# Kernel tuning notes

Hardware: AMD Instinct MI355X
Metric: run time of the kernel (lower is better)

## Reference

```python
import jax, jax.numpy as jnp
import numpy as np

H = 16  # num_heads
LN_EPS = 1e-5


def setup_inputs() -> dict:
    key = jax.random.key(0)
    ks = jax.random.split(key, 12)
    B, S, HS = 2, 1024, 1024
    D = HS // H
    vocab = 2 * 512 + 1  # 2*max_relative_position + 1
    inp = {
        "q": jax.random.normal(ks[0], (B, S, HS), jnp.float32),
        "k": jax.random.normal(ks[1], (B, S, HS), jnp.float32),
        "v": jax.random.normal(ks[2], (B, S, HS), jnp.float32),
        "rel_positions": jax.random.randint(ks[3], (S, S), 0, vocab, jnp.int64),
        "Wq": jax.random.normal(ks[4], (HS, HS), jnp.float32) * 0.02,
        "bq": jnp.zeros((HS,), jnp.float32),
        "Wk": jax.random.normal(ks[5], (HS, HS), jnp.float32) * 0.02,
        "bk": jnp.zeros((HS,), jnp.float32),
        "Wv": jax.random.normal(ks[6], (HS, HS), jnp.float32) * 0.02,
        "bv": jnp.zeros((HS,), jnp.float32),
        "rel_key_emb": jax.random.normal(ks[7], (vocab, D), jnp.float32) * 0.02,
        "rel_val_emb": jax.random.normal(ks[8], (vocab, D), jnp.float32) * 0.02,
        "Wo": jax.random.normal(ks[9], (HS, HS), jnp.float32) * 0.02,
        "bo": jnp.zeros((HS,), jnp.float32),
        "ln_g": jnp.ones((HS,), jnp.float32),
        "ln_b": jnp.zeros((HS,), jnp.float32),
    }
    return inp


def _layer_norm(x, g, b):
    mu = jnp.mean(x, axis=-1, keepdims=True)
    var = jnp.mean(jnp.square(x - mu), axis=-1, keepdims=True)
    return (x - mu) * jax.lax.rsqrt(var + LN_EPS) * g + b


def reference(q, k, v, rel_positions, Wq, bq, Wk, bk, Wv, bv,
              rel_key_emb, rel_val_emb, Wo, bo, ln_g, ln_b):
    B, S, HS = q.shape
    D = HS // H
    residual = q
    # projections (torch Linear: x @ W^T + b), split heads -> (B,H,S,D)
    qh = (q @ Wq.T + bq).reshape(B, S, H, D).transpose(0, 2, 1, 3)
    kh = (k @ Wk.T + bk).reshape(B, S, H, D).transpose(0, 2, 1, 3)
    vh = (v @ Wv.T + bv).reshape(B, S, H, D).transpose(0, 2, 1, 3)
    # relative embeddings: (S,S,D)
    rk = rel_key_emb[rel_positions]
    rv = rel_val_emb[rel_positions]
    # logits: content + relative-key term (note: original has NO 1/sqrt(d) scaling)
    logits = jnp.einsum('bhqd,bhkd->bhqk', qh, kh) \
           + jnp.einsum('bhqd,qkd->bhqk', qh, rk)
    weights = jax.nn.softmax(logits, axis=-1)
    # output: content + relative-value term
    ctx = jnp.einsum('bhqk,bhkd->bhqd', weights, vh) \
        + jnp.einsum('bhqk,qkd->bhqd', weights, rv)
    out = ctx.transpose(0, 2, 1, 3).reshape(B, S, HS) @ Wo.T + bo
    out = _layer_norm(out + residual, ln_g, ln_b)
    return (out, weights)
```

## Files before the change

### kernel.cpp

```cpp
#include <hip/hip_runtime.h>
#include <hip/hip_bf16.h>
#include <stdint.h>

#define B_   2
#define S_   1024
#define HS_  1024
#define H_   16
#define D_   64
#define V_   1025
#define VP_  1056
#define BH_  32
#define RTS_S 1072
#define RVS_  66

typedef __attribute__((ext_vector_type(8))) short  short8;
typedef __attribute__((ext_vector_type(4))) short  short4v;
typedef __attribute__((ext_vector_type(4))) float  floatx4;
typedef __attribute__((ext_vector_type(4))) int    intx4;
typedef __bf16 bf16x8 __attribute__((ext_vector_type(8)));

__device__ inline short f2b(float f) {
  union { float f; uint32_t u; } c; c.f = f;
  uint32_t u = c.u;
  uint32_t r = (u + 0x7fffu + ((u >> 16) & 1u)) >> 16;
  return (short)r;
}
__device__ inline float b2f(short s) {
  union { uint32_t u; float f; } c; c.u = ((uint32_t)(uint16_t)s) << 16;
  return c.f;
}
__device__ inline short8 cvt8(const float* p) {
  const floatx4* p4 = reinterpret_cast<const floatx4*>(p);
  floatx4 x = p4[0], y = p4[1];
  short8 r;
  r[0]=f2b(x[0]); r[1]=f2b(x[1]); r[2]=f2b(x[2]); r[3]=f2b(x[3]);
  r[4]=f2b(y[0]); r[5]=f2b(y[1]); r[6]=f2b(y[2]); r[7]=f2b(y[3]);
  return r;
}
__device__ inline short8 load_s8(const short* p) {
  return *reinterpret_cast<const short8*>(p);
}
__device__ inline floatx4 mfma16(short8 a, short8 b, floatx4 c) {
  return __builtin_amdgcn_mfma_f32_16x16x32_bf16(
      __builtin_bit_cast(bf16x8, a), __builtin_bit_cast(bf16x8, b), c, 0, 0, 0);
}

__global__ __launch_bounds__(256) void k_prep(const float* __restrict__ rve,
                                              const float* __restrict__ rke,
                                              short* __restrict__ rveB,
                                              short* __restrict__ rkeB) {
  int idx = blockIdx.x * 256 + threadIdx.x;
  if (idx < V_ * D_) {
    rveB[idx] = f2b(rve[idx]);
  } else {
    int j = idx - V_ * D_;
    if (j < V_ * D_) rkeB[j] = f2b(rke[j]);
  }
}

__global__ __launch_bounds__(256) void k_proj(
    const float* __restrict__ qi, const float* __restrict__ ki, const float* __restrict__ vi,
    const float* __restrict__ Wq, const float* __restrict__ bq,
    const float* __restrict__ Wk, const float* __restrict__ bk,
    const float* __restrict__ Wv, const float* __restrict__ bv,
    short* __restrict__ qh, short* __restrict__ kh, short* __restrict__ vhT) {
  int which = blockIdx.z;
  const float* X = which == 0 ? qi : which == 1 ? ki : vi;
  const float* W = which == 0 ? Wq : which == 1 ? Wk : Wv;
  const float* bias = which == 0 ? bq : which == 1 ? bk : bv;
  int m0 = blockIdx.y * 64, n0 = blockIdx.x * 64;
  int tid = threadIdx.x, wave = tid >> 6, lane = tid & 63;
  int qd = lane >> 4, c16 = lane & 15;
  __shared__ short Wl[64][40];
  floatx4 acc[4] = {};
  int mrow = m0 + wave * 16 + c16;
  const float* arow = X + (size_t)mrow * HS_ + qd * 8;
  int sn = tid >> 2, sk = (tid & 3) * 8;
  const float* wrow = W + (size_t)(n0 + sn) * HS_ + sk;
  for (int kc = 0; kc < HS_; kc += 32) {
    short8 wsv = cvt8(wrow + kc);
    *reinterpret_cast<short8*>(&Wl[sn][sk]) = wsv;
    __syncthreads();
    short8 a = cvt8(arow + kc);
#pragma unroll
    for (int nt = 0; nt < 4; nt++) {
      short8 b = *reinterpret_cast<const short8*>(&Wl[nt * 16 + c16][qd * 8]);
      acc[nt] = mfma16(a, b, acc[nt]);
    }
    __syncthreads();
  }
#pragma unroll
  for (int nt = 0; nt < 4; nt++) {
    int col = n0 + nt * 16 + c16;
    float bsum = bias[col];
    if (which < 2) {
      short* dst = which == 0 ? qh : kh;
#pragma unroll
      for (int r = 0; r < 4; r++) {
        int row = m0 + wave * 16 + qd * 4 + r;
        dst[(size_t)row * HS_ + col] = f2b(acc[nt][r] + bsum);
      }
    } else {
      int h = col >> 6, d = col & 63;
      int srow = m0 + wave * 16 + qd * 4;
      int bb = srow >> 10, s = srow & 1023;
      short4v pk;
#pragma unroll
      for (int r = 0; r < 4; r++) pk[r] = f2b(acc[nt][r] + bsum);
      *reinterpret_cast<short4v*>(&vhT[(((size_t)(bb * H_ + h)) * D_ + d) * S_ + s]) = pk;
    }
  }
}

__global__ __launch_bounds__(256, 4) void k_score(
    const short* __restrict__ qh, const short* __restrict__ kh,
    const short* __restrict__ rkeB, const int* __restrict__ rp,
    float* __restrict__ weights) {
  int bh = blockIdx.y;
  int b = bh >> 4, h = bh & 15;
  int q0 = blockIdx.x * 16;
  int tid = threadIdx.x, wave = tid >> 6, lane = tid & 63;
  int qd = lane >> 4, c16 = lane & 15;
  __shared__ short Rt[16 * RTS_S];
  __shared__ float redA[4 * 16];
  __shared__ float redB[4 * 16];

  const short* aptr = qh + ((size_t)b * S_ + q0 + c16) * HS_ + h * 64 + qd * 8;
  short8 a0 = load_s8(aptr), a1 = load_s8(aptr + 32);

  for (int nt = wave; nt < VP_ / 16; nt += 4) {
    int p = nt * 16 + c16;
    short8 b0 = {}, b1 = {};
    if (p < V_) {
      b0 = load_s8(rkeB + (size_t)p * D_ + qd * 8);
      b1 = load_s8(rkeB + (size_t)p * D_ + 32 + qd * 8);
    }
    floatx4 acc = {};
    acc = mfma16(a0, b0, acc);
    acc = mfma16(a1, b1, acc);
#pragma unroll
    for (int r = 0; r < 4; r++) Rt[(qd * 4 + r) * RTS_S + p] = f2b(acc[r]);
  }
  __syncthreads();

  floatx4 acc[16];
  const int* rpq = rp + (size_t)q0 * S_;
#pragma unroll
  for (int it = 0; it < 16; it++) {
    int col = wave * 256 + it * 16 + c16;
    const short* bptr = kh + ((size_t)b * S_ + col) * HS_ + h * 64 + qd * 8;
    floatx4 a = {};
    a = mfma16(a0, load_s8(bptr), a);
    a = mfma16(a1, load_s8(bptr + 32), a);
#pragma unroll
    for (int r = 0; r < 4; r++) {
      int row = qd * 4 + r;
      int p = rpq[(size_t)row * S_ + col];
      a[r] += b2f(Rt[row * RTS_S + p]);
    }
    acc[it] = a;
  }

  float mx[4], inv[4];
#pragma unroll
  for (int r = 0; r < 4; r++) {
    float m = -1e30f;
#pragma unroll
    for (int it = 0; it < 16; it++) m = fmaxf(m, acc[it][r]);
#pragma unroll
    for (int off = 1; off < 16; off <<= 1) m = fmaxf(m, __shfl_xor(m, off));
    mx[r] = m;
    if (c16 == 0) redA[wave * 16 + qd * 4 + r] = m;
  }
  __syncthreads();
#pragma unroll
  for (int r = 0; r < 4; r++) {
    int row = qd * 4 + r;
    float m = fmaxf(fmaxf(redA[row], redA[16 + row]),
                    fmaxf(redA[32 + row], redA[48 + row]));
    mx[r] = m;
  }
  float sm[4] = {0.f, 0.f, 0.f, 0.f};
#pragma unroll
  for (int it = 0; it < 16; it++) {
#pragma unroll
    for (int r = 0; r < 4; r++) {
      float e = __expf(acc[it][r] - mx[r]);
      acc[it][r] = e;
      sm[r] += e;
    }
  }
#pragma unroll
  for (int r = 0; r < 4; r++) {
#pragma unroll
    for (int off = 1; off < 16; off <<= 1) sm[r] += __shfl_xor(sm[r], off);
    if (c16 == 0) redB[wave * 16 + qd * 4 + r] = sm[r];
  }
  __syncthreads();
#pragma unroll
  for (int r = 0; r < 4; r++) {
    int row = qd * 4 + r;
    inv[r] = 1.f / (redB[row] + redB[16 + row] + redB[32 + row] + redB[48 + row]);
  }

  float* wout = weights + (size_t)bh * S_ * S_ + (size_t)q0 * S_;
#pragma unroll
  for (int it = 0; it < 16; it++) {
    int col = wave * 256 + it * 16 + c16;
#pragma unroll
    for (int r = 0; r < 4; r++) {
      wout[(size_t)(qd * 4 + r) * S_ + col] = acc[it][r] * inv[r];
    }
  }
}

__global__ __launch_bounds__(256, 4) void k_relgemm(
    const float* __restrict__ weights, const int* __restrict__ rp,
    const short* __restrict__ rveB, float* __restrict__ ctx_rel) {
  int q = blockIdx.x;
  int tid = threadIdx.x, wave = tid >> 6, lane = tid & 63;
  int qd = lane >> 4, c16 = lane & 15;
  __shared__ int   rpl[S_];
  __shared__ short Wl[32][40];
  __shared__ short Rv[32][RVS_];

  {
    const intx4* r4 = reinterpret_cast<const intx4*>(rp + (size_t)q * S_);
    reinterpret_cast<intx4*>(rpl)[tid] = r4[tid];
  }
  __syncthreads();

  int sn = tid >> 3;
  int sk = (tid & 7) * 4;
  int part = tid & 7;
  const float* wbase = weights + ((size_t)sn * S_ + q) * S_;
  floatx4 acc0 = {}, acc1 = {};
  int d0 = wave * 16;

  for (int kc = 0; kc < S_; kc += 32) {
    {
      floatx4 wv = *reinterpret_cast<const floatx4*>(wbase + kc + sk);
      short4v pk;
      pk[0] = f2b(wv[0]); pk[1] = f2b(wv[1]);
      pk[2] = f2b(wv[2]); pk[3] = f2b(wv[3]);
      *reinterpret_cast<short4v*>(&Wl[sn][sk]) = pk;
    }
    {
      int p = rpl[kc + sn];
      *reinterpret_cast<short8*>(&Rv[sn][part * 8]) =
          load_s8(rveB + (size_t)p * D_ + part * 8);
    }
    __syncthreads();
    short8 a0 = *reinterpret_cast<const short8*>(&Wl[c16][qd * 8]);
    short8 a1 = *reinterpret_cast<const short8*>(&Wl[16 + c16][qd * 8]);
    short8 bfr;
#pragma unroll
    for (int j = 0; j < 8; j++) bfr[j] = Rv[qd * 8 + j][d0 + c16];
    acc0 = mfma16(a0, bfr, acc0);
    acc1 = mfma16(a1, bfr, acc1);
    __syncthreads();
  }

  int dd = d0 + c16;
#pragma unroll
  for (int r = 0; r < 4; r++) {
    int bh0 = qd * 4 + r;
    int bh1 = 16 + bh0;
    ctx_rel[((size_t)0 * S_ + q) * HS_ + bh0 * 64 + dd] = acc0[r];
    ctx_rel[((size_t)1 * S_ + q) * HS_ + bh0 * 64 + dd] = acc1[r];
  }
}

__global__ __launch_bounds__(256, 4) void k_ctx2(
    const float* __restrict__ weights, const short* __restrict__ vhT,
    const float* __restrict__ ctx_rel, short* __restrict__ ctx) {
  int bh = blockIdx.y;
  int b = bh >> 4, h = bh & 15;
  int q0 = blockIdx.x * 32;
  int tid = threadIdx.x, wave = tid >> 6, lane = tid & 63;
  int qd = lane >> 4, c16 = lane & 15;
  int mt = wave >> 1;
  int dh = wave & 1;
  __shared__ short Vl[64][40];
  floatx4 acc[2] = {};
  const float* arow = weights + ((size_t)bh * S_ + q0 + mt * 16 + c16) * S_ + qd * 8;
  int sd = tid >> 2, sk = (tid & 3) * 8;
  const short* vrow = vhT + ((size_t)bh * D_ + sd) * S_ + sk;
  for (int kc = 0; kc < S_; kc += 32) {
    *reinterpret_cast<short8*>(&Vl[sd][sk]) = load_s8(vrow + kc);
    __syncthreads();
    short8 a = cvt8(arow + kc);
#pragma unroll
    for (int nt = 0; nt < 2; nt++) {
      short8 bfr = *reinterpret_cast<const short8*>(&Vl[dh * 32 + nt * 16 + c16][qd * 8]);
      acc[nt] = mfma16(a, bfr, acc[nt]);
    }
    __syncthreads();
  }
#pragma unroll
  for (int nt = 0; nt < 2; nt++) {
    int d = dh * 32 + nt * 16 + c16;
#pragma unroll
    for (int r = 0; r < 4; r++) {
      int q = q0 + mt * 16 + qd * 4 + r;
      size_t off = ((size_t)b * S_ + q) * HS_ + h * 64 + d;
      ctx[off] = f2b(acc[nt][r] + ctx_rel[off]);
    }
  }
}

__global__ __launch_bounds__(256) void k_oproj(
    const short* __restrict__ ctx, const float* __restrict__ Wo,
    const float* __restrict__ bo, float* __restrict__ out0) {
  int m0 = blockIdx.y * 64, n0 = blockIdx.x * 64;
  int tid = threadIdx.x, wave = tid >> 6, lane = tid & 63;
  int qd = lane >> 4, c16 = lane & 15;
  __shared__ short Wl[64][40];
  floatx4 acc[4] = {};
  const short* arow = ctx + (size_t)(m0 + wave * 16 + c16) * HS_ + qd * 8;
  int sn = tid >> 2, sk = (tid & 3) * 8;
  const float* wrow = Wo + (size_t)(n0 + sn) * HS_ + sk;
  for (int kc = 0; kc < HS_; kc += 32) {
    short8 wsv = cvt8(wrow + kc);
    *reinterpret_cast<short8*>(&Wl[sn][sk]) = wsv;
    __syncthreads();
    short8 a = load_s8(arow + kc);
#pragma unroll
    for (int nt = 0; nt < 4; nt++) {
      short8 b = *reinterpret_cast<const short8*>(&Wl[nt * 16 + c16][qd * 8]);
      acc[nt] = mfma16(a, b, acc[nt]);
    }
    __syncthreads();
  }
#pragma unroll
  for (int nt = 0; nt < 4; nt++) {
    int col = n0 + nt * 16 + c16;
    float bsum = bo[col];
#pragma unroll
    for (int r = 0; r < 4; r++) {
      int row = m0 + wave * 16 + qd * 4 + r;
      out0[(size_t)row * HS_ + col] = acc[nt][r] + bsum;
    }
  }
}

__global__ __launch_bounds__(256) void k_ln(
    const float* __restrict__ out0, const float* __restrict__ resid,
    const float* __restrict__ g, const float* __restrict__ bb,
    float* __restrict__ out) {
  int row = blockIdx.x;
  int tid = threadIdx.x, wave = tid >> 6, lane = tid & 63;
  const floatx4* x4 = reinterpret_cast<const floatx4*>(out0 + (size_t)row * HS_);
  const floatx4* r4 = reinterpret_cast<const floatx4*>(resid + (size_t)row * HS_);
  floatx4 x = x4[tid] + r4[tid];
  float s = x[0] + x[1] + x[2] + x[3];
  float ss = x[0]*x[0] + x[1]*x[1] + x[2]*x[2] + x[3]*x[3];
  __shared__ float red[8];
#pragma unroll
  for (int off = 32; off > 0; off >>= 1) {
    s += __shfl_xor(s, off);
    ss += __shfl_xor(ss, off);
  }
  if (lane == 0) { red[wave] = s; red[wave + 4] = ss; }
  __syncthreads();
  s = red[0] + red[1] + red[2] + red[3];
  ss = red[4] + red[5] + red[6] + red[7];
  float mu = s * (1.f / 1024.f);
  float var = ss * (1.f / 1024.f) - mu * mu;
  float rs = rsqrtf(var + 1e-5f);
  int c = tid * 4;
  floatx4 gg = *reinterpret_cast<const floatx4*>(g + c);
  floatx4 bv = *reinterpret_cast<const floatx4*>(bb + c);
  floatx4 y = (x - mu) * rs * gg + bv;
  reinterpret_cast<floatx4*>(out + (size_t)row * HS_)[tid] = y;
}

extern "C" void kernel_launch(void* const* d_in, const int* in_sizes, int n_in,
                              void* d_out, int out_size, void* d_ws, size_t ws_size,
                              hipStream_t stream) {
  const float* q   = (const float*)d_in[0];
  const float* k   = (const float*)d_in[1];
  const float* v   = (const float*)d_in[2];
  const int*   rp  = (const int*)d_in[3];
  const float* Wq  = (const float*)d_in[4];
  const float* bq  = (const float*)d_in[5];
  const float* Wk  = (const float*)d_in[6];
  const float* bk  = (const float*)d_in[7];
  const float* Wv  = (const float*)d_in[8];
  const float* bv  = (const float*)d_in[9];
  const float* rke = (const float*)d_in[10];
  const float* rve = (const float*)d_in[11];
  const float* Wo  = (const float*)d_in[12];
  const float* bo  = (const float*)d_in[13];
  const float* lng = (const float*)d_in[14];
  const float* lnb = (const float*)d_in[15];

  float* out = (float*)d_out;
  float* weights = out + (size_t)B_ * S_ * HS_;

  char* ws = (char*)d_ws;
  short* qh      = (short*)(ws);
  short* kh      = (short*)(ws + 4194304);
  short* vhT     = (short*)(ws + 8388608);
  short* ctx     = (short*)(ws + 12582912);
  short* rveB    = (short*)(ws + 16777216);
  short* rkeB    = (short*)(ws + 16912384);
  float* ctx_rel = (float*)(ws + 17043968);
  float* out0    = (float*)(ws + 25432576);

  k_prep    <<<dim3(513),        256, 0, stream>>>(rve, rke, rveB, rkeB);
  k_proj    <<<dim3(16, 32, 3),  256, 0, stream>>>(q, k, v, Wq, bq, Wk, bk, Wv, bv, qh, kh, vhT);
  k_score   <<<dim3(64, 32),     256, 0, stream>>>(qh, kh, rkeB, rp, weights);
  k_relgemm <<<dim3(1024),       256, 0, stream>>>(weights, rp, rveB, ctx_rel);
  k_ctx2    <<<dim3(32, 32),     256, 0, stream>>>(weights, vhT, ctx_rel, ctx);
  k_oproj   <<<dim3(16, 32),     256, 0, stream>>>(ctx, Wo, bo, out0);
  k_ln      <<<dim3(2048),       256, 0, stream>>>(out0, q, lng, lnb, out);
}
```

Baseline: 447.7 us.

## Pre-convert inputs and weights to bf16 and use 2x2-wave tiled GEMMs

Adds a k_cvt kernel that converts q/k/v and all four weight matrices to bf16 once, so the projection and output GEMMs read bf16 instead of converting fp32 in their inner loops. k_proj, k_ctx2 and k_oproj are rewritten to stage both A and B tiles in shared memory, with a 2x2 wave arrangement giving each wave a 32x32 output tile for more operand reuse. The cost is an extra launch and extra workspace traffic for the converted copies, and k_ctx2 now launches half as many blocks. A small index cleanup in k_relgemm does not change its behaviour.

```diff
diff --git a/kernel.cpp b/kernel.cpp
--- a/kernel.cpp
+++ b/kernel.cpp
@@ -58,58 +58,75 @@
   }
 }
 
-__global__ __launch_bounds__(256) void k_proj(
-    const float* __restrict__ qi, const float* __restrict__ ki, const float* __restrict__ vi,
-    const float* __restrict__ Wq, const float* __restrict__ bq,
-    const float* __restrict__ Wk, const float* __restrict__ bk,
-    const float* __restrict__ Wv, const float* __restrict__ bv,
+__global__ __launch_bounds__(256) void k_cvt(
+    const float* __restrict__ q, const float* __restrict__ k, const float* __restrict__ v,
+    const float* __restrict__ Wq, const float* __restrict__ Wk,
+    const float* __restrict__ Wv, const float* __restrict__ Wo,
+    short* __restrict__ xb, short* __restrict__ wb) {
+  int z = blockIdx.z;
+  const float* src = z == 0 ? q : z == 1 ? k : z == 2 ? v
+                   : z == 3 ? Wq : z == 4 ? Wk : z == 5 ? Wv : Wo;
+  int n = (z < 3) ? (1 << 21) : (1 << 20);
+  short* dst = (z < 3) ? xb + (size_t)z * (1 << 21) : wb + (size_t)(z - 3) * (1 << 20);
+  int i = (blockIdx.x * 256 + threadIdx.x) * 8;
+  if (i < n) *reinterpret_cast<short8*>(&dst[i]) = cvt8(src + i);
+}
+
+
+__global__ __launch_bounds__(256, 4) void k_proj(
+    const short* __restrict__ xb, const short* __restrict__ wb,
+    const float* __restrict__ bq, const float* __restrict__ bk, const float* __restrict__ bv,
     short* __restrict__ qh, short* __restrict__ kh, short* __restrict__ vhT) {
   int which = blockIdx.z;
-  const float* X = which == 0 ? qi : which == 1 ? ki : vi;
-  const float* W = which == 0 ? Wq : which == 1 ? Wk : Wv;
+  const short* A  = xb + (size_t)which * (2048u * 1024u);
+  const short* Bm = wb + (size_t)which * (1024u * 1024u);
   const float* bias = which == 0 ? bq : which == 1 ? bk : bv;
-  int m0 = blockIdx.y * 64, n0 = blockIdx.x * 64;
-  int tid = threadIdx.x, wave = tid >> 6, lane = tid & 63;
-  int qd = lane >> 4, c16 = lane & 15;
-  __shared__ short Wl[64][40];
-  floatx4 acc[4] = {};
-  int mrow = m0 + wave * 16 + c16;
-  const float* arow = X + (size_t)mrow * HS_ + qd * 8;
-  int sn = tid >> 2, sk = (tid & 3) * 8;
-  const float* wrow = W + (size_t)(n0 + sn) * HS_ + sk;
-  for (int kc = 0; kc < HS_; kc += 32) {
-    short8 wsv = cvt8(wrow + kc);
-    *reinterpret_cast<short8*>(&Wl[sn][sk]) = wsv;
-    __syncthreads();
-    short8 a = cvt8(arow + kc);
-#pragma unroll
-    for (int nt = 0; nt < 4; nt++) {
-      short8 b = *reinterpret_cast<const short8*>(&Wl[nt * 16 + c16][qd * 8]);
-      acc[nt] = mfma16(a, b, acc[nt]);
-    }
-    __syncthreads();
-  }
-#pragma unroll
-  for (int nt = 0; nt < 4; nt++) {
-    int col = n0 + nt * 16 + c16;
-    float bsum = bias[col];
-    if (which < 2) {
-      short* dst = which == 0 ? qh : kh;
-#pragma unroll
-      for (int r = 0; r < 4; r++) {
-        int row = m0 + wave * 16 + qd * 4 + r;
-        dst[(size_t)row * HS_ + col] = f2b(acc[nt][r] + bsum);
+  int m0 = blockIdx.x * 64, n0 = blockIdx.y * 64;
+  int tid = threadIdx.x, wid = tid >> 6, lane = tid & 63;
+  int wr = wid >> 1, wc = wid & 1, qd = lane >> 4, c16 = lane & 15;
+  __shared__ short As[4 * 64 * 8];
+  __shared__ short Bs[4 * 64 * 8];
+  int kk = tid & 3, rowi = tid >> 2;
+  const short* ga = A  + (size_t)(m0 + rowi) * HS_ + kk * 8;
+  const short* gb = Bm + (size_t)(n0 + rowi) * HS_ + kk * 8;
+  floatx4 acc[2][2] = {};
+  for (int k0 = 0; k0 < HS_; k0 += 32) {
+    short8 av = load_s8(ga + k0);
+    short8 bv8 = load_s8(gb + k0);
+    __syncthreads();
+    *reinterpret_cast<short8*>(&As[kk * 512 + rowi * 8]) = av;
+    *reinterpret_cast<short8*>(&Bs[kk * 512 + rowi * 8]) = bv8;
+    __syncthreads();
+    short8 a0 = load_s8(&As[qd * 512 + (wr * 32 + c16) * 8]);
+    short8 a1 = load_s8(&As[qd * 512 + (wr * 32 + 16 + c16) * 8]);
+    short8 b0 = load_s8(&Bs[qd * 512 + (wc * 32 + c16) * 8]);
+    short8 b1 = load_s8(&Bs[qd * 512 + (wc * 32 + 16 + c16) * 8]);
+    acc[0][0] = mfma16(a0, b0, acc[0][0]);
+    acc[0][1] = mfma16(a0, b1, acc[0][1]);
+    acc[1][0] = mfma16(a1, b0, acc[1][0]);
+    acc[1][1] = mfma16(a1, b1, acc[1][1]);
+  }
+#pragma unroll
+  for (int mi = 0; mi < 2; mi++)
+#pragma unroll
+    for (int ni = 0; ni < 2; ni++) {
+      int col = n0 + wc * 32 + ni * 16 + c16;
+      float bs = bias[col];
+      int gr0 = m0 + wr * 32 + mi * 16 + qd * 4;
+      if (which < 2) {
+        short* dst = which == 0 ? qh : kh;
+#pragma unroll
+        for (int r = 0; r < 4; r++)
+          dst[(size_t)(gr0 + r) * HS_ + col] = f2b(acc[mi][ni][r] + bs);
+      } else {
+        int h = col >> 6, d = col & 63;
+        int bb = gr0 >> 10, s = gr0 & 1023;
+        short4v pk;
+#pragma unroll
+        for (int r = 0; r < 4; r++) pk[r] = f2b(acc[mi][ni][r] + bs);
+        *reinterpret_cast<short4v*>(&vhT[(((size_t)(bb * H_ + h)) * D_ + d) * S_ + s]) = pk;
       }
-    } else {
-      int h = col >> 6, d = col & 63;
-      int srow = m0 + wave * 16 + qd * 4;
-      int bb = srow >> 10, s = srow & 1023;
-      short4v pk;
-#pragma unroll
-      for (int r = 0; r < 4; r++) pk[r] = f2b(acc[nt][r] + bsum);
-      *reinterpret_cast<short4v*>(&vhT[(((size_t)(bb * H_ + h)) * D_ + d) * S_ + s]) = pk;
-    }
-  }
+    }
 }
 
 __global__ __launch_bounds__(256, 4) void k_score(
@@ -231,7 +248,7 @@
   __syncthreads();
 
   int sn = tid >> 3;
-  int sk = (tid & 7) * 4;
+  int sk = (tid & 3) * 8;
   int part = tid & 7;
   const float* wbase = weights + ((size_t)sn * S_ + q) * S_;
   floatx4 acc0 = {}, acc1 = {};
@@ -239,11 +256,12 @@
 
   for (int kc = 0; kc < S_; kc += 32) {
     {
-      floatx4 wv = *reinterpret_cast<const floatx4*>(wbase + kc + sk);
+      int skA = (tid & 7) * 4;
+      floatx4 wv = *reinterpret_cast<const floatx4*>(wbase + kc + skA);
       short4v pk;
       pk[0] = f2b(wv[0]); pk[1] = f2b(wv[1]);
       pk[2] = f2b(wv[2]); pk[3] = f2b(wv[3]);
-      *reinterpret_cast<short4v*>(&Wl[sn][sk]) = pk;
+      *reinterpret_cast<short4v*>(&Wl[sn][skA]) = pk;
     }
     {
       int p = rpl[kc + sn];
@@ -265,7 +283,6 @@
 #pragma unroll
   for (int r = 0; r < 4; r++) {
     int bh0 = qd * 4 + r;
-    int bh1 = 16 + bh0;
     ctx_rel[((size_t)0 * S_ + q) * HS_ + bh0 * 64 + dd] = acc0[r];
     ctx_rel[((size_t)1 * S_ + q) * HS_ + bh0 * 64 + dd] = acc1[r];
   }
@@ -276,72 +293,84 @@
     const float* __restrict__ ctx_rel, short* __restrict__ ctx) {
   int bh = blockIdx.y;
   int b = bh >> 4, h = bh & 15;
-  int q0 = blockIdx.x * 32;
-  int tid = threadIdx.x, wave = tid >> 6, lane = tid & 63;
-  int qd = lane >> 4, c16 = lane & 15;
-  int mt = wave >> 1;
-  int dh = wave & 1;
-  __shared__ short Vl[64][40];
-  floatx4 acc[2] = {};
-  const float* arow = weights + ((size_t)bh * S_ + q0 + mt * 16 + c16) * S_ + qd * 8;
-  int sd = tid >> 2, sk = (tid & 3) * 8;
-  const short* vrow = vhT + ((size_t)bh * D_ + sd) * S_ + sk;
-  for (int kc = 0; kc < S_; kc += 32) {
-    *reinterpret_cast<short8*>(&Vl[sd][sk]) = load_s8(vrow + kc);
-    __syncthreads();
-    short8 a = cvt8(arow + kc);
-#pragma unroll
-    for (int nt = 0; nt < 2; nt++) {
-      short8 bfr = *reinterpret_cast<const short8*>(&Vl[dh * 32 + nt * 16 + c16][qd * 8]);
-      acc[nt] = mfma16(a, bfr, acc[nt]);
-    }
-    __syncthreads();
-  }
-#pragma unroll
-  for (int nt = 0; nt < 2; nt++) {
-    int d = dh * 32 + nt * 16 + c16;
-#pragma unroll
-    for (int r = 0; r < 4; r++) {
-      int q = q0 + mt * 16 + qd * 4 + r;
-      size_t off = ((size_t)b * S_ + q) * HS_ + h * 64 + d;
-      ctx[off] = f2b(acc[nt][r] + ctx_rel[off]);
-    }
-  }
-}
-
-__global__ __launch_bounds__(256) void k_oproj(
-    const short* __restrict__ ctx, const float* __restrict__ Wo,
+  int m0 = blockIdx.x * 64;
+  int tid = threadIdx.x, wid = tid >> 6, lane = tid & 63;
+  int wr = wid >> 1, wc = wid & 1, qd = lane >> 4, c16 = lane & 15;
+  __shared__ short As[4 * 64 * 8];
+  __shared__ short Bs[4 * 64 * 8];
+  int kk = tid & 3, rowi = tid >> 2;
+  const float* gaf = weights + (size_t)bh * S_ * S_ + (size_t)(m0 + rowi) * S_ + kk * 8;
+  const short* gb  = vhT + ((size_t)bh * D_ + rowi) * S_ + kk * 8;
+  floatx4 acc[2][2] = {};
+  for (int k0 = 0; k0 < S_; k0 += 32) {
+    short8 av = cvt8(gaf + k0);
+    short8 bv8 = load_s8(gb + k0);
+    __syncthreads();
+    *reinterpret_cast<short8*>(&As[kk * 512 + rowi * 8]) = av;
+    *reinterpret_cast<short8*>(&Bs[kk * 512 + rowi * 8]) = bv8;
+    __syncthreads();
+    short8 a0 = load_s8(&As[qd * 512 + (wr * 32 + c16) * 8]);
+    short8 a1 = load_s8(&As[qd * 512 + (wr * 32 + 16 + c16) * 8]);
+    short8 b0 = load_s8(&Bs[qd * 512 + (wc * 32 + c16) * 8]);
+    short8 b1 = load_s8(&Bs[qd * 512 + (wc * 32 + 16 + c16) * 8]);
+    acc[0][0] = mfma16(a0, b0, acc[0][0]);
+    acc[0][1] = mfma16(a0, b1, acc[0][1]);
+    acc[1][0] = mfma16(a1, b0, acc[1][0]);
+    acc[1][1] = mfma16(a1, b1, acc[1][1]);
+  }
+#pragma unroll
+  for (int mi = 0; mi < 2; mi++)
+#pragma unroll
+    for (int ni = 0; ni < 2; ni++) {
+      int d = wc * 32 + ni * 16 + c16;
+      int gq0 = m0 + wr * 32 + mi * 16 + qd * 4;
+#pragma unroll
+      for (int r = 0; r < 4; r++) {
+        size_t off = ((size_t)b * S_ + gq0 + r) * HS_ + h * 64 + d;
+        ctx[off] = f2b(acc[mi][ni][r] + ctx_rel[off]);
+      }
+    }
+}
+
+__global__ __launch_bounds__(256, 4) void k_oproj(
+    const short* __restrict__ ctx, const short* __restrict__ wob,
     const float* __restrict__ bo, float* __restrict__ out0) {
-  int m0 = blockIdx.y * 64, n0 = blockIdx.x * 64;
-  int tid = threadIdx.x, wave = tid >> 6, lane = tid & 63;
-  int qd = lane >> 4, c16 = lane & 15;
-  __shared__ short Wl[64][40];
-  floatx4 acc[4] = {};
-  const short* arow = ctx + (size_t)(m0 + wave * 16 + c16) * HS_ + qd * 8;
-  int sn = tid >> 2, sk = (tid & 3) * 8;
-  const float* wrow = Wo + (size_t)(n0 + sn) * HS_ + sk;
-  for (int kc = 0; kc < HS_; kc += 32) {
-    short8 wsv = cvt8(wrow + kc);
-    *reinterpret_cast<short8*>(&Wl[sn][sk]) = wsv;
-    __syncthreads();
-    short8 a = load_s8(arow + kc);
-#pragma unroll
-    for (int nt = 0; nt < 4; nt++) {
-      short8 b = *reinterpret_cast<const short8*>(&Wl[nt * 16 + c16][qd * 8]);
-      acc[nt] = mfma16(a, b, acc[nt]);
-    }
-    __syncthreads();
-  }
-#pragma unroll
-  for (int nt = 0; nt < 4; nt++) {
-    int col = n0 + nt * 16 + c16;
-    float bsum = bo[col];
-#pragma unroll
-    for (int r = 0; r < 4; r++) {
-      int row = m0 + wave * 16 + qd * 4 + r;
-      out0[(size_t)row * HS_ + col] = acc[nt][r] + bsum;
-    }
-  }
+  int m0 = blockIdx.x * 64, n0 = blockIdx.y * 64;
+  int tid = threadIdx.x, wid = tid >> 6, lane = tid & 63;
+  int wr = wid >> 1, wc = wid & 1, qd = lane >> 4, c16 = lane & 15;
+  __shared__ short As[4 * 64 * 8];
+  __shared__ short Bs[4 * 64 * 8];
+  int kk = tid & 3, rowi = tid >> 2;
+  const short* ga = ctx + (size_t)(m0 + rowi) * HS_ + kk * 8;
+  const short* gb = wob + (size_t)(n0 + rowi) * HS_ + kk * 8;
+  floatx4 acc[2][2] = {};
+  for (int k0 = 0; k0 < HS_; k0 += 32) {
+    short8 av = load_s8(ga + k0);
+    short8 bv8 = load_s8(gb + k0);
+    __syncthreads();
+    *reinterpret_cast<short8*>(&As[kk * 512 + rowi * 8]) = av;
+    *reinterpret_cast<short8*>(&Bs[kk * 512 + rowi * 8]) = bv8;
+    __syncthreads();
+    short8 a0 = load_s8(&As[qd * 512 + (wr * 32 + c16) * 8]);
+    short8 a1 = load_s8(&As[qd * 512 + (wr * 32 + 16 + c16) * 8]);
+    short8 b0 = load_s8(&Bs[qd * 512 + (wc * 32 + c16) * 8]);
+    short8 b1 = load_s8(&Bs[qd * 512 + (wc * 32 + 16 + c16) * 8]);
+    acc[0][0] = mfma16(a0, b0, acc[0][0]);
+    acc[0][1] = mfma16(a0, b1, acc[0][1]);
+    acc[1][0] = mfma16(a1, b0, acc[1][0]);
+    acc[1][1] = mfma16(a1, b1, acc[1][1]);
+  }
+#pragma unroll
+  for (int mi = 0; mi < 2; mi++)
+#pragma unroll
+    for (int ni = 0; ni < 2; ni++) {
+      int col = n0 + wc * 32 + ni * 16 + c16;
+      float bs = bo[col];
+      int gr0 = m0 + wr * 32 + mi * 16 + qd * 4;
+#pragma unroll
+      for (int r = 0; r < 4; r++)
+        out0[(size_t)(gr0 + r) * HS_ + col] = acc[mi][ni][r] + bs;
+    }
 }
 
 __global__ __launch_bounds__(256) void k_ln(
@@ -407,12 +436,16 @@
   short* rkeB    = (short*)(ws + 16912384);
   float* ctx_rel = (float*)(ws + 17043968);
   float* out0    = (float*)(ws + 25432576);
+  short* xb      = (short*)(ws + 33821184);
+  short* wb      = (short*)(ws + 46404096);
+  short* wob     = wb + (size_t)3 * (1 << 20);
 
   k_prep    <<<dim3(513),        256, 0, stream>>>(rve, rke, rveB, rkeB);
-  k_proj    <<<dim3(16, 32, 3),  256, 0, stream>>>(q, k, v, Wq, bq, Wk, bk, Wv, bv, qh, kh, vhT);
+  k_cvt     <<<dim3(1024, 1, 7), 256, 0, stream>>>(q, k, v, Wq, Wk, Wv, Wo, xb, wb);
+  k_proj    <<<dim3(32, 16, 3),  256, 0, stream>>>(xb, wb, bq, bk, bv, qh, kh, vhT);
   k_score   <<<dim3(64, 32),     256, 0, stream>>>(qh, kh, rkeB, rp, weights);
   k_relgemm <<<dim3(1024),       256, 0, stream>>>(weights, rp, rveB, ctx_rel);
-  k_ctx2    <<<dim3(32, 32),     256, 0, stream>>>(weights, vhT, ctx_rel, ctx);
-  k_oproj   <<<dim3(16, 32),     256, 0, stream>>>(ctx, Wo, bo, out0);
+  k_ctx2    <<<dim3(16, 32),     256, 0, stream>>>(weights, vhT, ctx_rel, ctx);
+  k_oproj   <<<dim3(32, 16),     256, 0, stream>>>(ctx, wob, bo, out0);
   k_ln      <<<dim3(2048),       256, 0, stream>>>(out0, q, lng, lnb, out);
 }
```

After: 414.9 us. 7.3% less time.
